# Performance work log

Hardware: AMD Instinct MI355X
Metric: run time of the kernel (lower is better)

## Reference

```python
import jax, jax.numpy as jnp
import numpy as np

B, T, C, H = 2, 2048, 1024, 16
D = C // H  # head_dim = 64


def _ln(x, g, b, eps=1e-5):
    mu = x.mean(-1, keepdims=True)
    var = ((x - mu) ** 2).mean(-1, keepdims=True)
    return (x - mu) / jnp.sqrt(var + eps) * g + b


def _lif_rate(I, tau_rc=0.02, tau_ref=0.002, v_th=1.0, eps=1e-7):
    good = I > v_th + eps
    I_safe = jnp.where(good, I, v_th + 1.0)  # avoid log1p(<=-1)
    r = 1.0 / (tau_ref - tau_rc * jnp.log1p(-v_th / I_safe))
    return jnp.where(good, r, 0.0)


def setup_inputs() -> dict:
    key = jax.random.key(0)
    ks = jax.random.split(key, 12)
    w = lambda k, shp: jax.random.normal(k, shp, dtype=jnp.float32) * 0.02
    enc = jax.random.normal(ks[9], (H, T, D), dtype=jnp.float32)
    enc_hat = enc / jnp.maximum(jnp.linalg.norm(enc, axis=-1, keepdims=True), 1e-8)
    return {
        "x": jax.random.normal(ks[0], (B, T, C), dtype=jnp.float32),
        "ln1_g": jnp.ones((C,), jnp.float32), "ln1_b": jnp.zeros((C,), jnp.float32),
        "qkv_w": w(ks[1], (C, 3 * C)), "qkv_b": jnp.zeros((3 * C,), jnp.float32),
        "out_w": w(ks[2], (C, C)), "out_b": jnp.zeros((C,), jnp.float32),
        "ln2_g": jnp.ones((C,), jnp.float32), "ln2_b": jnp.zeros((C,), jnp.float32),
        "mlp_w1": w(ks[3], (C, 4 * C)), "mlp_b1": jnp.zeros((4 * C,), jnp.float32),
        "mlp_w2": w(ks[4], (4 * C, C)), "mlp_b2": jnp.zeros((C,), jnp.float32),
        "enc_hat": enc_hat,
        "gain": jax.random.uniform(ks[10], (1, H, T, 1), dtype=jnp.float32) * 200.0,
        "bias_attn": jax.random.uniform(ks[11], (1, H, T, 1), dtype=jnp.float32),
    }


def reference(x, ln1_g, ln1_b, qkv_w, qkv_b, out_w, out_b,
              ln2_g, ln2_b, mlp_w1, mlp_b1, mlp_w2, mlp_b2,
              enc_hat, gain, bias_attn):
    b, t, c = x.shape
    x_norm = _ln(x, ln1_g, ln1_b)
    qkv = x_norm @ qkv_w + qkv_b                      # [B,T,3C]
    qkv = qkv.reshape(b, t, 3, H, D).transpose(2, 0, 3, 1, 4)
    Q, K_unused, V = qkv[0], qkv[1], qkv[2]           # each [B,H,T,D]; K unused (matches source)
    E = enc_hat[:, :t, :]
    G = gain[:, :, :t, :]
    BIAS = bias_attn[:, :, :t, :]
    I = G * jnp.einsum('bhtd,hsd->bhts', Q, E) + BIAS  # [B,H,T,T]
    scores = _lif_rate(I) / jnp.sqrt(jnp.float32(D))
    causal = jnp.tril(jnp.ones((t, t), dtype=bool))[None, None]
    scores = jnp.where(causal, scores, -jnp.inf)
    attn_w = jax.nn.softmax(scores, axis=-1)
    attn_out = jnp.einsum('bhts,bhsd->bhtd', attn_w, V)
    attn_out = attn_out.transpose(0, 2, 1, 3).reshape(b, t, c)
    x = x + attn_out @ out_w + out_b
    h = _ln(x, ln2_g, ln2_b)
    h = jax.nn.gelu(h @ mlp_w1 + mlp_b1, approximate=False) @ mlp_w2 + mlp_b2
    return x + h
```

## Files before the change

### kernel.cpp

```cpp
#include <hip/hip_runtime.h>
#include <math.h>

#define Bdim 2
#define Tdim 2048
#define Cdim 1024
#define Hdim 16
#define Ddim 64

typedef unsigned short u16;
typedef __attribute__((ext_vector_type(8))) short bf16x8;
typedef __attribute__((ext_vector_type(4))) float f32x4;

__device__ __forceinline__ float b2f(u16 s){
  union { float f; unsigned u; } v; v.u = ((unsigned)s) << 16; return v.f;
}
__device__ __forceinline__ u16 f2b(float f){
  union { float f; unsigned u; } v; v.f = f;
  unsigned r = v.u + 0x7fffu + ((v.u >> 16) & 1u);
  return (u16)(r >> 16);
}
__device__ __forceinline__ float loadf(const void* p, size_t i, int bf){
  float r;
  if(bf) r = b2f(((const u16*)p)[i]);
  else   r = ((const float*)p)[i];
  return r;
}
__device__ __forceinline__ f32x4 mfma16(bf16x8 a, bf16x8 b, f32x4 c){
  return __builtin_amdgcn_mfma_f32_16x16x32_bf16(a, b, c, 0, 0, 0);
}

__global__ void detect_k(const u16* __restrict__ x, int* __restrict__ flag){
  if(threadIdx.x == 0 && blockIdx.x == 0){
    int sane = 0;
    for(int i = 0; i < 64; i++){
      int e = (x[i] >> 7) & 0xFF;
      sane += (e == 0 || (e >= 0x6E && e <= 0x8A)) ? 1 : 0;
    }
    *flag = (sane >= 56) ? 1 : 0;
  }
}

__global__ __launch_bounds__(256) void cvt_k(const void* __restrict__ in,
    u16* __restrict__ out, int n, const int* __restrict__ flagp){
  int bf = *flagp;
  int i = blockIdx.x * 256 + threadIdx.x;
  if(i < n) out[i] = bf ? ((const u16*)in)[i] : f2b(((const float*)in)[i]);
}

__global__ __launch_bounds__(256) void transpose_k(const void* __restrict__ in,
    u16* __restrict__ out, int K, int N, const int* __restrict__ flagp){
  __shared__ u16 tile[32][34];
  int bf = *flagp;
  int n0 = blockIdx.x * 32, k0 = blockIdx.y * 32;
  int tx = threadIdx.x & 31, ty = threadIdx.x >> 5;
  #pragma unroll
  for(int i = 0; i < 4; i++)
    tile[ty + i*8][tx] = f2b(loadf(in, (size_t)(k0 + ty + i*8) * N + n0 + tx, bf));
  __syncthreads();
  #pragma unroll
  for(int i = 0; i < 4; i++)
    out[(size_t)(n0 + ty + i*8) * K + k0 + tx] = tile[tx][ty + i*8];
}

template<int SRC>
__global__ __launch_bounds__(256) void ln_k(const void* __restrict__ xin,
    const void* __restrict__ g, const void* __restrict__ be,
    u16* __restrict__ out, const int* __restrict__ flagp){
  __shared__ float red[256];
  int bf = *flagp;
  int row = blockIdx.x, t = threadIdx.x;
  float v[4]; float s = 0.f;
  #pragma unroll
  for(int i = 0; i < 4; i++){
    size_t idx = (size_t)row * Cdim + t + i*256;
    v[i] = (SRC == 1) ? ((const float*)xin)[idx] : loadf(xin, idx, bf);
    s += v[i];
  }
  red[t] = s; __syncthreads();
  for(int o = 128; o > 0; o >>= 1){ if(t < o) red[t] += red[t+o]; __syncthreads(); }
  float mu = red[0] * (1.f / Cdim);
  __syncthreads();
  s = 0.f;
  #pragma unroll
  for(int i = 0; i < 4; i++){ float d = v[i] - mu; s += d*d; }
  red[t] = s; __syncthreads();
  for(int o = 128; o > 0; o >>= 1){ if(t < o) red[t] += red[t+o]; __syncthreads(); }
  float rstd = rsqrtf(red[0] * (1.f / Cdim) + 1e-5f);
  u16* orow = out + (size_t)row * Cdim;
  #pragma unroll
  for(int i = 0; i < 4; i++){
    int c = t + i*256;
    orow[c] = f2b((v[i] - mu) * rstd * loadf(g, c, bf) + loadf(be, c, bf));
  }
}

enum { EPI_QKV = 0, EPI_RES = 1, EPI_GELU = 2, EPI_FINAL = 3 };

template<int EPI, int KK>
__global__ __launch_bounds__(256) void gemm_k(
    const u16* __restrict__ A, const u16* __restrict__ Bt, const void* __restrict__ bias,
    void* __restrict__ out0, void* __restrict__ out1, const void* __restrict__ res,
    int M, int N, int mofs, const int* __restrict__ flagp)
{
  const int K = KK;
  __shared__ u16 As[128 * 72];
  __shared__ u16 Bs[128 * 72];
  int bf = *flagp;
  int tid = threadIdx.x;
  int m0 = blockIdx.y * 128, n0 = blockIdx.x * 128;
  int w = tid >> 6, l = tid & 63;
  int lq = l & 15, lk = l >> 4;
  int m_off = (w & 1) * 64, n_off = (w >> 1) * 64;
  int srow = tid >> 3;
  int scol = (tid & 7) * 8;
  int br[4], ar[4];
  #pragma unroll
  for(int i = 0; i < 4; i++){
    ar[i] = m0 + srow + 32*i;
    br[i] = n0 + srow + 32*i;
    if(EPI == EPI_QKV && br[i] >= 1024) br[i] += 1024;
  }
  f32x4 acc[4][4] = {};
  for(int k0 = 0; k0 < K; k0 += 64){
    bf16x8 av[4], bv[4];
    #pragma unroll
    for(int i = 0; i < 4; i++)
      av[i] = *(const bf16x8*)(A  + (size_t)ar[i] * K + k0 + scol);
    #pragma unroll
    for(int i = 0; i < 4; i++)
      bv[i] = *(const bf16x8*)(Bt + (size_t)br[i] * K + k0 + scol);
    __syncthreads();
    #pragma unroll
    for(int i = 0; i < 4; i++)
      *(bf16x8*)&As[(srow + 32*i) * 72 + scol] = av[i];
    #pragma unroll
    for(int i = 0; i < 4; i++)
      *(bf16x8*)&Bs[(srow + 32*i) * 72 + scol] = bv[i];
    __syncthreads();
    #pragma unroll
    for(int kk = 0; kk < 2; kk++){
      bf16x8 af[4], bfr[4];
      #pragma unroll
      for(int mb = 0; mb < 4; mb++)
        af[mb]  = *(const bf16x8*)&As[(m_off + mb*16 + lq) * 72 + kk*32 + lk*8];
      #pragma unroll
      for(int nb = 0; nb < 4; nb++)
        bfr[nb] = *(const bf16x8*)&Bs[(n_off + nb*16 + lq) * 72 + kk*32 + lk*8];
      #pragma unroll
      for(int mb = 0; mb < 4; mb++)
        #pragma unroll
        for(int nb = 0; nb < 4; nb++)
          acc[mb][nb] = mfma16(af[mb], bfr[nb], acc[mb][nb]);
    }
  }
  #pragma unroll
  for(int mb = 0; mb < 4; mb++)
  #pragma unroll
  for(int nb = 0; nb < 4; nb++){
    #pragma unroll
    for(int r = 0; r < 4; r++){
      int m = m0 + m_off + mb*16 + lk*4 + r;
      int n = n0 + n_off + nb*16 + lq;
      float v = acc[mb][nb][r];
      if(EPI == EPI_QKV){
        int bsrc = (n < 1024) ? n : n + 1024;
        v += loadf(bias, bsrc, bf);
        int bb = m / Tdim, t = m % Tdim;
        if(n < 1024){
          int h = n >> 6, d = n & 63;
          ((u16*)out0)[(((size_t)(bb*Hdim + h)*Tdim + t) << 6) + d] = f2b(v);
        } else {
          int nv = n - 1024; int h = nv >> 6, d = nv & 63;
          ((u16*)out1)[((size_t)(bb*Hdim + h)*Ddim + d)*Tdim + t] = f2b(v);
        }
      } else if(EPI == EPI_RES){
        v += loadf(bias, n, bf) + loadf(res, (size_t)m*N + n, bf);
        ((float*)out0)[(size_t)m*N + n] = v;
      } else if(EPI == EPI_GELU){
        v += loadf(bias, n, bf);
        float gl = 0.5f * v * (1.0f + erff(v * 0.70710678118f));
        ((u16*)out0)[(size_t)m*N + n] = f2b(gl);
      } else {
        v += loadf(bias, n, bf) + ((const float*)res)[(size_t)m*N + n];
        size_t oi = (size_t)(mofs + m) * N + n;
        if(bf) ((u16*)out0)[oi] = f2b(v);
        else   ((float*)out0)[oi] = v;
      }
    }
  }
}

__global__ __launch_bounds__(64) void attn_k(
    const u16* __restrict__ Q, const u16* __restrict__ Vt, const u16* __restrict__ E,
    const void* __restrict__ gain, const void* __restrict__ battn,
    u16* __restrict__ aout, const int* __restrict__ flagp)
{
  __shared__ u16 P[16][72];
  int bf = *flagp;
  int rt = 127 - (int)(blockIdx.x >> 5), bh = blockIdx.x & 31;
  int b = bh >> 4, h = bh & 15;
  int l = threadIdx.x & 63;
  int lq = l & 15, lk = l >> 4;
  const u16* Qb = Q  + (size_t)bh * Tdim * Ddim;
  const u16* Vb = Vt + (size_t)bh * Ddim * Tdim;
  const u16* Eh = E  + (size_t)h  * Tdim * Ddim;
  int qrow = rt * 16;
  int stmax = rt >> 2;
  bf16x8 qf[2];
  #pragma unroll
  for(int ks = 0; ks < 2; ks++)
    qf[ks] = *(const bf16x8*)(Qb + (size_t)(qrow + lq) * Ddim + ks*32 + lk*8);
  float g4[4], b4[4];
  #pragma unroll
  for(int r = 0; r < 4; r++){
    int t = qrow + lk*4 + r;
    g4[r] = loadf(gain, h * Tdim + t, bf);
    b4[r] = loadf(battn, h * Tdim + t, bf);
  }
  bf16x8 onesf;
  #pragma unroll
  for(int j = 0; j < 8; j++) onesf[j] = (short)0x3F80;
  f32x4 num[4] = {};
  f32x4 den4 = {0.f, 0.f, 0.f, 0.f};
  for(int st = 0; st <= stmax; st++){
    f32x4 sc[4] = {};
    #pragma unroll
    for(int ks = 0; ks < 2; ks++){
      #pragma unroll
      for(int nb = 0; nb < 4; nb++){
        bf16x8 ef = *(const bf16x8*)(Eh + (size_t)(st*64 + nb*16 + lq) * Ddim + ks*32 + lk*8);
        sc[nb] = mfma16(qf[ks], ef, sc[nb]);
      }
    }
    #pragma unroll
    for(int nb = 0; nb < 4; nb++){
      #pragma unroll
      for(int r = 0; r < 4; r++){
        int sg = st*64 + nb*16 + lq;
        int qg = qrow + lk*4 + r;
        float I = fmaf(g4[r], sc[nb][r], b4[r]);
        float u = (I - 1.0f) * __builtin_amdgcn_rcpf(I);
        float L = __builtin_amdgcn_logf(u);
        float denom = fmaf(-0.013862944f, L, 0.002f);
        float e = __builtin_amdgcn_exp2f(0.18033688f * __builtin_amdgcn_rcpf(denom));
        float p = (I > 1.0000001f) ? e : 1.0f;
        p = (sg <= qg) ? p : 0.f;
        P[lk*4 + r][nb*16 + lq] = f2b(p);
      }
    }
    #pragma unroll
    for(int ks = 0; ks < 2; ks++){
      bf16x8 pf = *(const bf16x8*)&P[lq][ks*32 + lk*8];
      den4 = mfma16(pf, onesf, den4);
      #pragma unroll
      for(int nb = 0; nb < 4; nb++){
        bf16x8 vf = *(const bf16x8*)(Vb + (size_t)(nb*16 + lq) * Tdim + st*64 + ks*32 + lk*8);
        num[nb] = mfma16(pf, vf, num[nb]);
      }
    }
  }
  float rden[4];
  #pragma unroll
  for(int r = 0; r < 4; r++) rden[r] = __builtin_amdgcn_rcpf(den4[r]);
  #pragma unroll
  for(int nb = 0; nb < 4; nb++){
    #pragma unroll
    for(int r = 0; r < 4; r++){
      int t = qrow + lk*4 + r;
      int d = nb*16 + lq;
      float o = num[nb][r] * rden[r];
      aout[((size_t)b * Tdim + t) * Cdim + h * Ddim + d] = f2b(o);
    }
  }
}

extern "C" void kernel_launch(void* const* d_in, const int* in_sizes, int n_in,
                              void* d_out, int out_size, void* d_ws, size_t ws_size,
                              hipStream_t stream)
{
  const void* x      = d_in[0];
  const void* ln1_g  = d_in[1];
  const void* ln1_b  = d_in[2];
  const void* qkv_w  = d_in[3];
  const void* qkv_b  = d_in[4];
  const void* out_w  = d_in[5];
  const void* out_b  = d_in[6];
  const void* ln2_g  = d_in[7];
  const void* ln2_b  = d_in[8];
  const void* mlp_w1 = d_in[9];
  const void* mlp_b1 = d_in[10];
  const void* mlp_w2 = d_in[11];
  const void* mlp_b2 = d_in[12];
  const void* enc    = d_in[13];
  const void* gain   = d_in[14];
  const void* battn  = d_in[15];
  (void)in_sizes; (void)n_in; (void)out_size;

  const size_t MB = 1024 * 1024;
  char* ws = (char*)d_ws;
  int*   flag = (int*)(ws);
  u16*   R0   = (u16*)(ws + 256);
  u16*   R1   = (u16*)(ws + 256 + 8*MB);
  float* x2   = (float*)(ws + 256 + 16*MB);
  u16*   R3a  = (u16*)(ws + 256 + 32*MB);
  u16*   R3b  = (u16*)(ws + 256 + 40*MB);
  u16*   Ebf  = (u16*)(ws + 256 + 48*MB);
  u16*   gbuf = (u16*)(ws + 256 + 52*MB);
  bool fullM = ws_size >= 85*MB;

  dim3 blk(256);
  detect_k<<<1, 64, 0, stream>>>((const u16*)x, flag);
  ln_k<0><<<4096, blk, 0, stream>>>(x, ln1_g, ln1_b, R0, flag);
  transpose_k<<<dim3(3072/32, 1024/32), blk, 0, stream>>>(qkv_w, R1, 1024, 3072, flag);
  cvt_k<<<(Hdim*Tdim*Ddim)/256, blk, 0, stream>>>(enc, Ebf, Hdim*Tdim*Ddim, flag);
  gemm_k<EPI_QKV,1024><<<dim3(2048/128, 4096/128), blk, 0, stream>>>(
      R0, R1, qkv_b, R3a, R3b, nullptr, 4096, 2048, 0, flag);
  attn_k<<<dim3(32*128), dim3(64), 0, stream>>>(R3a, R3b, Ebf, gain, battn, R0, flag);
  transpose_k<<<dim3(1024/32, 1024/32), blk, 0, stream>>>(out_w, R1, 1024, 1024, flag);
  gemm_k<EPI_RES,1024><<<dim3(1024/128, 4096/128), blk, 0, stream>>>(
      R0, R1, out_b, x2, nullptr, x, 4096, 1024, 0, flag);
  ln_k<1><<<4096, blk, 0, stream>>>(x2, ln2_g, ln2_b, R3a, flag);
  transpose_k<<<dim3(4096/32, 1024/32), blk, 0, stream>>>(mlp_w1, R0, 1024, 4096, flag);
  transpose_k<<<dim3(1024/32, 4096/32), blk, 0, stream>>>(mlp_w2, R1, 4096, 1024, flag);
  if(fullM){
    gemm_k<EPI_GELU,1024><<<dim3(4096/128, 4096/128), blk, 0, stream>>>(
        R3a, R0, mlp_b1, gbuf, nullptr, nullptr, 4096, 4096, 0, flag);
    gemm_k<EPI_FINAL,4096><<<dim3(1024/128, 4096/128), blk, 0, stream>>>(
        gbuf, R1, mlp_b2, d_out, nullptr, x2, 4096, 1024, 0, flag);
  } else {
    for(int q = 0; q < 4; q++){
      int ro = q * 1024;
      gemm_k<EPI_GELU,1024><<<dim3(4096/128, 1024/128), blk, 0, stream>>>(
          R3a + (size_t)ro*1024, R0, mlp_b1, R3b, nullptr, nullptr, 1024, 4096, 0, flag);
      gemm_k<EPI_FINAL,4096><<<dim3(1024/128, 1024/128), blk, 0, stream>>>(
          R3b, R1, mlp_b2, d_out, nullptr, x2 + (size_t)ro*1024, 1024, 1024, ro, flag);
    }
  }
}
```

Before: 543.4 us.

## Split attention key tiles across two waves with shared-memory reduction

The attention kernel now runs two wavefronts per block. Each wave handles alternating 64-key tiles, and the partial numerators and denominators are combined through shared memory before the final normalized write. This doubles the parallelism per query tile, aimed at latency-bound long causal rows and better load balance. The causal mask is now applied only on the diagonal tile. In exchange it adds LDS usage, a block barrier and a reduction step.

```diff
diff --git a/kernel.cpp b/kernel.cpp
--- a/kernel.cpp
+++ b/kernel.cpp
@@ -190,16 +190,18 @@
   }
 }
 
-__global__ __launch_bounds__(64) void attn_k(
+__global__ __launch_bounds__(128, 8) void attn_k(
     const u16* __restrict__ Q, const u16* __restrict__ Vt, const u16* __restrict__ E,
     const void* __restrict__ gain, const void* __restrict__ battn,
     u16* __restrict__ aout, const int* __restrict__ flagp)
 {
-  __shared__ u16 P[16][72];
+  __shared__ u16 P[2][16][72];
+  __shared__ float red[64][21];
   int bf = *flagp;
   int rt = 127 - (int)(blockIdx.x >> 5), bh = blockIdx.x & 31;
   int b = bh >> 4, h = bh & 15;
-  int l = threadIdx.x & 63;
+  int w = (int)(threadIdx.x >> 6);
+  int l = (int)(threadIdx.x & 63);
   int lq = l & 15, lk = l >> 4;
   const u16* Qb = Q  + (size_t)bh * Tdim * Ddim;
   const u16* Vb = Vt + (size_t)bh * Ddim * Tdim;
@@ -222,7 +224,7 @@
   for(int j = 0; j < 8; j++) onesf[j] = (short)0x3F80;
   f32x4 num[4] = {};
   f32x4 den4 = {0.f, 0.f, 0.f, 0.f};
-  for(int st = 0; st <= stmax; st++){
+  for(int st = w; st <= stmax; st += 2){
     f32x4 sc[4] = {};
     #pragma unroll
     for(int ks = 0; ks < 2; ks++){
@@ -232,6 +234,7 @@
         sc[nb] = mfma16(qf[ks], ef, sc[nb]);
       }
     }
+    int diag = (st == stmax);
     #pragma unroll
     for(int nb = 0; nb < 4; nb++){
       #pragma unroll
@@ -244,13 +247,13 @@
         float denom = fmaf(-0.013862944f, L, 0.002f);
         float e = __builtin_amdgcn_exp2f(0.18033688f * __builtin_amdgcn_rcpf(denom));
         float p = (I > 1.0000001f) ? e : 1.0f;
-        p = (sg <= qg) ? p : 0.f;
-        P[lk*4 + r][nb*16 + lq] = f2b(p);
+        if(diag) p = (sg <= qg) ? p : 0.f;
+        P[w][lk*4 + r][nb*16 + lq] = f2b(p);
       }
     }
     #pragma unroll
     for(int ks = 0; ks < 2; ks++){
-      bf16x8 pf = *(const bf16x8*)&P[lq][ks*32 + lk*8];
+      bf16x8 pf = *(const bf16x8*)&P[w][lq][ks*32 + lk*8];
       den4 = mfma16(pf, onesf, den4);
       #pragma unroll
       for(int nb = 0; nb < 4; nb++){
@@ -259,17 +262,35 @@
       }
     }
   }
-  float rden[4];
-  #pragma unroll
-  for(int r = 0; r < 4; r++) rden[r] = __builtin_amdgcn_rcpf(den4[r]);
-  #pragma unroll
-  for(int nb = 0; nb < 4; nb++){
-    #pragma unroll
-    for(int r = 0; r < 4; r++){
-      int t = qrow + lk*4 + r;
-      int d = nb*16 + lq;
-      float o = num[nb][r] * rden[r];
-      aout[((size_t)b * Tdim + t) * Cdim + h * Ddim + d] = f2b(o);
+  if(w == 1){
+    #pragma unroll
+    for(int nb = 0; nb < 4; nb++)
+      #pragma unroll
+      for(int r = 0; r < 4; r++)
+        red[l][nb*4 + r] = num[nb][r];
+    #pragma unroll
+    for(int r = 0; r < 4; r++) red[l][16 + r] = den4[r];
+  }
+  __syncthreads();
+  if(w == 0){
+    #pragma unroll
+    for(int nb = 0; nb < 4; nb++)
+      #pragma unroll
+      for(int r = 0; r < 4; r++)
+        num[nb][r] += red[l][nb*4 + r];
+    float rden[4];
+    #pragma unroll
+    for(int r = 0; r < 4; r++)
+      rden[r] = __builtin_amdgcn_rcpf(den4[r] + red[l][16 + r]);
+    #pragma unroll
+    for(int nb = 0; nb < 4; nb++){
+      #pragma unroll
+      for(int r = 0; r < 4; r++){
+        int t = qrow + lk*4 + r;
+        int d = nb*16 + lq;
+        float o = num[nb][r] * rden[r];
+        aout[((size_t)b * Tdim + t) * Cdim + h * Ddim + d] = f2b(o);
+      }
     }
   }
 }
@@ -315,7 +336,7 @@
   cvt_k<<<(Hdim*Tdim*Ddim)/256, blk, 0, stream>>>(enc, Ebf, Hdim*Tdim*Ddim, flag);
   gemm_k<EPI_QKV,1024><<<dim3(2048/128, 4096/128), blk, 0, stream>>>(
       R0, R1, qkv_b, R3a, R3b, nullptr, 4096, 2048, 0, flag);
-  attn_k<<<dim3(32*128), dim3(64), 0, stream>>>(R3a, R3b, Ebf, gain, battn, R0, flag);
+  attn_k<<<dim3(32*128), dim3(128), 0, stream>>>(R3a, R3b, Ebf, gain, battn, R0, flag);
   transpose_k<<<dim3(1024/32, 1024/32), blk, 0, stream>>>(out_w, R1, 1024, 1024, flag);
   gemm_k<EPI_RES,1024><<<dim3(1024/128, 4096/128), blk, 0, stream>>>(
       R0, R1, out_b, x2, nullptr, x, 4096, 1024, 0, flag);
```

Result: slower. 632.5 us (+16.4%).

## Share E and V tiles across four waves via double-buffered LDS in attention

Applied to the files above, without the earlier changes.

The attention kernel now runs 256-thread blocks with four waves, each handling a 16-row query tile of one 64-row block. The E and V key tiles are loaded once per block into double-buffered shared memory, with the next tile prefetched into registers while the current one is computed. The causal mask is applied only on the diagonal tile. This cuts redundant global loads of E and V by sharing them across waves, at the cost of block-wide syncs and more shared memory per block.

```diff
diff --git a/kernel.cpp b/kernel.cpp
--- a/kernel.cpp
+++ b/kernel.cpp
@@ -190,22 +190,28 @@
   }
 }
 
-__global__ __launch_bounds__(64) void attn_k(
+__global__ __launch_bounds__(256, 3) void attn_k(
     const u16* __restrict__ Q, const u16* __restrict__ Vt, const u16* __restrict__ E,
     const void* __restrict__ gain, const void* __restrict__ battn,
     u16* __restrict__ aout, const int* __restrict__ flagp)
 {
-  __shared__ u16 P[16][72];
-  int bf = *flagp;
-  int rt = 127 - (int)(blockIdx.x >> 5), bh = blockIdx.x & 31;
+  __shared__ u16 Es[2][64][72];
+  __shared__ u16 Vs[2][64][72];
+  __shared__ u16 P[4][16][72];
+  int bf = *flagp;
+  int k  = 31 - (int)(blockIdx.x >> 5);
+  int bh = blockIdx.x & 31;
   int b = bh >> 4, h = bh & 15;
-  int l = threadIdx.x & 63;
+  int tid = threadIdx.x;
+  int w = tid >> 6, l = tid & 63;
   int lq = l & 15, lk = l >> 4;
+  int rt = k * 4 + w;
+  int qrow = rt * 16;
   const u16* Qb = Q  + (size_t)bh * Tdim * Ddim;
   const u16* Vb = Vt + (size_t)bh * Ddim * Tdim;
   const u16* Eh = E  + (size_t)h  * Tdim * Ddim;
-  int qrow = rt * 16;
-  int stmax = rt >> 2;
+  int srow = tid >> 3;
+  int scol = (tid & 7) * 8;
   bf16x8 qf[2];
   #pragma unroll
   for(int ks = 0; ks < 2; ks++)
@@ -222,16 +228,36 @@
   for(int j = 0; j < 8; j++) onesf[j] = (short)0x3F80;
   f32x4 num[4] = {};
   f32x4 den4 = {0.f, 0.f, 0.f, 0.f};
-  for(int st = 0; st <= stmax; st++){
+  {
+    bf16x8 e0 = *(const bf16x8*)(Eh + (size_t)(srow     ) * Ddim + scol);
+    bf16x8 e1 = *(const bf16x8*)(Eh + (size_t)(srow + 32) * Ddim + scol);
+    bf16x8 v0 = *(const bf16x8*)(Vb + (size_t)(srow     ) * Tdim + scol);
+    bf16x8 v1 = *(const bf16x8*)(Vb + (size_t)(srow + 32) * Tdim + scol);
+    *(bf16x8*)&Es[0][srow     ][scol] = e0;
+    *(bf16x8*)&Es[0][srow + 32][scol] = e1;
+    *(bf16x8*)&Vs[0][srow     ][scol] = v0;
+    *(bf16x8*)&Vs[0][srow + 32][scol] = v1;
+  }
+  __syncthreads();
+  for(int st = 0; st <= k; st++){
+    int cur = st & 1;
+    bf16x8 pe0, pe1, pv0, pv1;
+    if(st < k){
+      pe0 = *(const bf16x8*)(Eh + (size_t)((st+1)*64 + srow     ) * Ddim + scol);
+      pe1 = *(const bf16x8*)(Eh + (size_t)((st+1)*64 + srow + 32) * Ddim + scol);
+      pv0 = *(const bf16x8*)(Vb + (size_t)(srow     ) * Tdim + (st+1)*64 + scol);
+      pv1 = *(const bf16x8*)(Vb + (size_t)(srow + 32) * Tdim + (st+1)*64 + scol);
+    }
     f32x4 sc[4] = {};
     #pragma unroll
     for(int ks = 0; ks < 2; ks++){
       #pragma unroll
       for(int nb = 0; nb < 4; nb++){
-        bf16x8 ef = *(const bf16x8*)(Eh + (size_t)(st*64 + nb*16 + lq) * Ddim + ks*32 + lk*8);
+        bf16x8 ef = *(const bf16x8*)&Es[cur][nb*16 + lq][ks*32 + lk*8];
         sc[nb] = mfma16(qf[ks], ef, sc[nb]);
       }
     }
+    int diag = (st == k);
     #pragma unroll
     for(int nb = 0; nb < 4; nb++){
       #pragma unroll
@@ -244,19 +270,26 @@
         float denom = fmaf(-0.013862944f, L, 0.002f);
         float e = __builtin_amdgcn_exp2f(0.18033688f * __builtin_amdgcn_rcpf(denom));
         float p = (I > 1.0000001f) ? e : 1.0f;
-        p = (sg <= qg) ? p : 0.f;
-        P[lk*4 + r][nb*16 + lq] = f2b(p);
+        if(diag) p = (sg <= qg) ? p : 0.f;
+        P[w][lk*4 + r][nb*16 + lq] = f2b(p);
       }
     }
     #pragma unroll
     for(int ks = 0; ks < 2; ks++){
-      bf16x8 pf = *(const bf16x8*)&P[lq][ks*32 + lk*8];
+      bf16x8 pf = *(const bf16x8*)&P[w][lq][ks*32 + lk*8];
       den4 = mfma16(pf, onesf, den4);
       #pragma unroll
       for(int nb = 0; nb < 4; nb++){
-        bf16x8 vf = *(const bf16x8*)(Vb + (size_t)(nb*16 + lq) * Tdim + st*64 + ks*32 + lk*8);
+        bf16x8 vf = *(const bf16x8*)&Vs[cur][nb*16 + lq][ks*32 + lk*8];
         num[nb] = mfma16(pf, vf, num[nb]);
       }
+    }
+    if(st < k){
+      *(bf16x8*)&Es[cur^1][srow     ][scol] = pe0;
+      *(bf16x8*)&Es[cur^1][srow + 32][scol] = pe1;
+      *(bf16x8*)&Vs[cur^1][srow     ][scol] = pv0;
+      *(bf16x8*)&Vs[cur^1][srow + 32][scol] = pv1;
+      __syncthreads();
     }
   }
   float rden[4];
@@ -315,7 +348,7 @@
   cvt_k<<<(Hdim*Tdim*Ddim)/256, blk, 0, stream>>>(enc, Ebf, Hdim*Tdim*Ddim, flag);
   gemm_k<EPI_QKV,1024><<<dim3(2048/128, 4096/128), blk, 0, stream>>>(
       R0, R1, qkv_b, R3a, R3b, nullptr, 4096, 2048, 0, flag);
-  attn_k<<<dim3(32*128), dim3(64), 0, stream>>>(R3a, R3b, Ebf, gain, battn, R0, flag);
+  attn_k<<<dim3(32*32), dim3(256), 0, stream>>>(R3a, R3b, Ebf, gain, battn, R0, flag);
   transpose_k<<<dim3(1024/32, 1024/32), blk, 0, stream>>>(out_w, R1, 1024, 1024, flag);
   gemm_k<EPI_RES,1024><<<dim3(1024/128, 4096/128), blk, 0, stream>>>(
       R0, R1, out_b, x2, nullptr, x, 4096, 1024, 0, flag);
```

Result: faster. 468.8 us (-13.7%).
